# Kernel optimization log

Hardware: AMD Instinct MI355X
Metric: run time of the kernel (lower is better)

The kernel has to match this reference:

```python
import jax, jax.numpy as jnp
from jax import lax
import numpy as np

RNN = 512; FC = 512; COND = 128; FEAT = 80; NCLS = 256; HALF = RNN // 2
PAD = 2; SCALES = (5, 5, 11); MEL_T = 86  # -> 22550 output samples


def setup_inputs() -> dict:
    key = jax.random.key(0)
    ks = jax.random.split(key, 12)
    s = 0.05
    p = {"mels": jax.random.normal(ks[0], (1, FEAT, MEL_T), jnp.float32)}
    ch = FEAT
    for i, sc in enumerate(SCALES):
        k = 2 * sc + 1
        p[f"up_w{i}"] = jax.random.normal(ks[1 + i], (COND, ch, k), jnp.float32) * s
        p[f"up_b{i}"] = jnp.zeros((COND,), jnp.float32)
        ch = COND
    p["Wx"] = jax.random.normal(ks[4], (3 * RNN, 3 + COND), jnp.float32) * s
    p["bx"] = jnp.zeros((3 * RNN,), jnp.float32)
    p["Wh"] = jax.random.normal(ks[5], (3 * RNN, RNN), jnp.float32) * s
    p["bh"] = jnp.zeros((3 * RNN,), jnp.float32)
    p["O1w"] = jax.random.normal(ks[6], (FC, HALF), jnp.float32) * s
    p["O1b"] = jnp.zeros((FC,), jnp.float32)
    p["O2w"] = jax.random.normal(ks[7], (NCLS, FC), jnp.float32) * s
    p["O2b"] = jnp.zeros((NCLS,), jnp.float32)
    p["O3w"] = jax.random.normal(ks[8], (FC, HALF), jnp.float32) * s
    p["O3b"] = jnp.zeros((FC,), jnp.float32)
    p["O4w"] = jax.random.normal(ks[9], (NCLS, FC), jnp.float32) * s
    p["O4b"] = jnp.zeros((NCLS,), jnp.float32)
    return p


def _upsample(mels, ws, bs):
    # mels[:, :, excess_pad:-excess_pad] with excess_pad = PAD - 1 = 1
    x = mels[:, :, PAD - 1:-(PAD - 1)]
    for w, b, sc in zip(ws, bs, SCALES):
        k = 2 * sc + 1
        # ConvTranspose1d(stride=sc, kernel=k, padding=(3*sc-1)//2) as an
        # input-dilated conv: edge pad = k-1-torch_pad = (sc+1)//2
        e = k - 1 - (3 * sc - 1) // 2
        x = lax.conv_general_dilated(x, w, window_strides=(1,),
                                     padding=[(e, e)], lhs_dilation=(sc,),
                                     dimension_numbers=('NCH', 'OIH', 'NCH'))
        x = jax.nn.relu(x + b[None, :, None])
    return x[0, :, 1:-1].T  # [T, COND]


def _gru(inp, h, Wx, bx, Wh, bh):
    xg = Wx @ inp + bx
    hg = Wh @ h + bh
    xr, xz, xn = jnp.split(xg, 3)
    hr, hz, hn = jnp.split(hg, 3)
    r = jax.nn.sigmoid(xr + hr)
    z = jax.nn.sigmoid(xz + hz)
    n = jnp.tanh(xn + r * hn)
    return (1.0 - z) * n + z * h


def reference(mels, up_w0, up_b0, up_w1, up_b1, up_w2, up_b2,
              Wx, bx, Wh, bh, O1w, O1b, O2w, O2b, O3w, O3b, O4w, O4b):
    cond = _upsample(mels, (up_w0, up_w1, up_w2), (up_b0, up_b1, up_b2))
    zero = jnp.float32(0.0)

    def step(carry, m_t):
        h, c_val, f_val = carry
        # coarse pass: x = [c_{t-1}, f_{t-1}, 0]
        inp1 = jnp.concatenate([jnp.stack([c_val, f_val, zero]), m_t])
        h1 = _gru(inp1, h, Wx, bx, Wh, bh)
        oc = O2w @ jax.nn.relu(O1w @ h1[:HALF] + O1b) + O2b
        c_cat = jnp.argmax(oc).astype(jnp.float32)  # deterministic=True path
        c_new = c_cat / 127.5 - 1.0
        # fine pass: x = [c_{t-1}, f_{t-1}, c_t]
        inp2 = jnp.concatenate([jnp.stack([c_val, f_val, c_new]), m_t])
        h2 = _gru(inp2, h, Wx, bx, Wh, bh)
        of = O4w @ jax.nn.relu(O3w @ h2[HALF:] + O3b) + O4b
        f_cat = jnp.argmax(of).astype(jnp.float32)
        f_new = f_cat / 127.5 - 1.0
        sample = (c_cat * 256.0 + f_cat) / 32767.5 - 1.0
        return (h2, c_new, f_new), (sample, jnp.concatenate([oc, of]))

    init = (jnp.zeros((RNN,), jnp.float32), zero, zero)
    _, (samples, logits) = lax.scan(step, init, cond)
    return samples, logits  # [T], [T, 512]
```

## Files before the change

kernel.cpp:

```cpp
#include <hip/hip_runtime.h>
#include <math.h>

#define T_STEPS 22550
#define NWG 32
#define NTHR 256

typedef unsigned long long ull;

#define SL_H1   0
#define SL_O1   256
#define SL_AM1  768
#define SL_H2   800
#define SL_O3   1312
#define SL_AM2  1824
#define SL_END  1888

#define OF_SLOT  64
#define OF_AFTER (OF_SLOT + SL_END*2)
#define OF_BUFA  OF_AFTER
#define OF_BUFB  (OF_BUFA + 128*412)
#define OF_COND  (OF_BUFB + 128*2052)

__global__ void k_init(float* ws){
  int i = blockIdx.x*blockDim.x + threadIdx.x;
  ull* sl = (ull*)(ws + OF_SLOT);
  if (i < SL_END) __hip_atomic_store(&sl[i], 0ULL, __ATOMIC_RELAXED, __HIP_MEMORY_SCOPE_AGENT);
}

__global__ void k_upconv(const float* __restrict__ x, int instride, int inoff,
                         const float* __restrict__ w, const float* __restrict__ b,
                         float* __restrict__ y, int Cin, int Lin, int K, int sc, int e,
                         int Lout, int mode)
{
  int j = blockIdx.x*blockDim.x + threadIdx.x;
  int c = blockIdx.y;
  if (j >= Lout) return;
  float acc = b[c];
  int kstart = ((e - j) % sc + sc) % sc;
  for (int i = 0; i < Cin; ++i){
    const float* wci = w + (c*Cin + i)*K;
    const float* xi  = x + i*instride + inoff;
    for (int k = kstart; k < K; k += sc){
      int qd = j - e + k;
      if (qd >= 0){
        int qq = qd / sc;
        if (qq < Lin) acc += wci[k]*xi[qq];
      }
    }
  }
  acc = fmaxf(acc, 0.f);
  if (mode == 0) y[c*Lout + j] = acc;
  else { int t = j - 1; if (t >= 0 && t < T_STEPS) y[t*128 + c] = acc; }
}

__device__ __forceinline__ float sigm(float x){ return 1.f/(1.f + expf(-x)); }

__device__ __forceinline__ void pub64(ull* p, ull pk){
  (void)__hip_atomic_exchange(p, pk, __ATOMIC_RELAXED, __HIP_MEMORY_SCOPE_AGENT);
}
__device__ __forceinline__ ull ld64(ull* p){
  return __hip_atomic_load(p, __ATOMIC_RELAXED, __HIP_MEMORY_SCOPE_AGENT);
}
__device__ __forceinline__ float spin_data(ull* p, unsigned tag){
  ull pk = ld64(p);
  while ((unsigned)pk != tag) pk = ld64(p);
  return __uint_as_float((unsigned)(pk >> 32));
}
__device__ __forceinline__ ull spin_am(ull* p, unsigned tag){
  ull pk = ld64(p);
  while ((unsigned)(pk & 0xFFFFFFu) != tag) pk = ld64(p);
  return pk;
}
__device__ __forceinline__ ull pack_data(float v, unsigned tag){
  return ((ull)__float_as_uint(v) << 32) | (ull)tag;
}

__launch_bounds__(NTHR)
__global__ void k_wavernn(const float* __restrict__ Wx, const float* __restrict__ bx,
                          const float* __restrict__ Wh, const float* __restrict__ bh,
                          const float* __restrict__ O1w, const float* __restrict__ O1b,
                          const float* __restrict__ O2w, const float* __restrict__ O2b,
                          const float* __restrict__ O3w, const float* __restrict__ O3b,
                          const float* __restrict__ O4w, const float* __restrict__ O4b,
                          float* ws, float* __restrict__ out)
{
  __shared__ __align__(16) float h_s[512];
  __shared__ __align__(16) float m_s[128];
  __shared__ __align__(16) float h1c_s[256];
  __shared__ __align__(16) float o_s[512];
  __shared__ float hg_s[48], xgb_s[48], xg1_s[48];
  __shared__ float red_s[8], sc_s[8];
  __shared__ float wc0_s[48], wc1_s[48], wc2_s[48], bx_s[48], bh_s[48];

  const int tid = threadIdx.x, g = blockIdx.x;
  ull* sl = (ull*)(ws + OF_SLOT);
  const float* cond = ws + OF_COND;
  float* out_samp = out;
  float* out_log  = out + T_STEPS;

  if (tid < 48){
    int row = (tid>>4)*512 + g + 32*(tid&15);
    wc0_s[tid] = Wx[(size_t)row*131 + 0];
    wc1_s[tid] = Wx[(size_t)row*131 + 1];
    wc2_s[tid] = Wx[(size_t)row*131 + 2];
    bx_s[tid]  = bx[row];
    bh_s[tid]  = bh[row];
  }
  const int m16 = tid>>4, c16 = tid&15;
  const int rowO1 = g + 32*m16;
  float wO1r[16], wO3r[16];
  #pragma unroll
  for (int k=0;k<16;++k){
    wO1r[k] = O1w[(size_t)rowO1*256 + c16*16 + k];
    wO3r[k] = O3w[(size_t)rowO1*256 + c16*16 + k];
  }
  const float bO1r = O1b[rowO1], bO3r = O3b[rowO1];
  const int m8 = tid>>5, l32 = tid&31;
  const int row2 = g + 32*m8;
  float wO2r[16], wO4r[16];
  #pragma unroll
  for (int k=0;k<16;++k){
    wO2r[k] = O2w[(size_t)row2*512 + l32 + 32*k];
    wO4r[k] = O4w[(size_t)row2*512 + l32 + 32*k];
  }
  const float bO2 = O2b[row2], bO4 = O4b[row2];

  h_s[tid] = 0.f; h_s[tid+256] = 0.f;
  if (tid < 128) m_s[tid] = cond[tid];
  if (tid == 0){ sc_s[0] = 0.f; sc_s[1] = 0.f; }
  __syncthreads();

  #define COMPUTE_WX() do { \
    if (tid < 192){ \
      const int li_ = tid>>2, q_ = tid&3; \
      const int row_ = (li_>>4)*512 + g + 32*(li_&15); \
      const float* WxR = Wx + (size_t)row_*131 + 3; \
      float aX = 0.f; \
      _Pragma("unroll") \
      for (int kk=0; kk<32; ++kk){ \
        int f_ = q_*32 + ((kk + 8*q_) & 31); \
        aX += WxR[f_]*m_s[f_]; \
      } \
      aX += __shfl_xor(aX,1); aX += __shfl_xor(aX,2); \
      if (q_ == 0) xgb_s[li_] = aX + bx_s[li_]; \
    } } while(0)

  #define COMPUTE_WH() do { \
    if (tid < 192){ \
      const int li_ = tid>>2, q_ = tid&3; \
      const int row_ = (li_>>4)*512 + g + 32*(li_&15); \
      const float4* W4 = (const float4*)(Wh + (size_t)row_*512); \
      const float4* H4 = (const float4*)h_s; \
      float aH = 0.f; \
      _Pragma("unroll") \
      for (int kk=0; kk<32; ++kk){ \
        int f_ = q_*32 + ((kk + 2*q_) & 31); \
        float4 w = W4[f_], v = H4[f_]; \
        aH += w.x*v.x + w.y*v.y + w.z*v.z + w.w*v.w; \
      } \
      aH += __shfl_xor(aH,1); aH += __shfl_xor(aH,2); \
      if (q_ == 0) hg_s[li_] = aH + bh_s[li_]; \
    } } while(0)

  COMPUTE_WX();
  COMPUTE_WH();

  for (int t = 0; t < T_STEPS; ++t){
    const unsigned tag = (unsigned)(t + 1);
    __syncthreads();

    if (tid < 48) xg1_s[tid] = xgb_s[tid] + sc_s[0]*wc0_s[tid] + sc_s[1]*wc1_s[tid];
    if (tid < 128 && t + 1 < T_STEPS) m_s[tid] = cond[(size_t)(t+1)*128 + tid];
    __syncthreads();

    if (tid < 8){
      float r = sigm(xg1_s[tid]     + hg_s[tid]);
      float z = sigm(xg1_s[16+tid]  + hg_s[16+tid]);
      float n = tanhf(xg1_s[32+tid] + r*hg_s[32+tid]);
      float h1 = (1.f - z)*n + z*h_s[g + 32*tid];
      pub64(&sl[SL_H1 + g*8 + tid], pack_data(h1, tag));
    }
    h1c_s[tid] = spin_data(&sl[SL_H1 + (tid & 31)*8 + (tid >> 5)], tag);
    __syncthreads();

    {
      float acc = 0.f;
      #pragma unroll
      for (int k=0;k<16;++k) acc += wO1r[k]*h1c_s[c16*16 + k];
      acc += __shfl_xor(acc,1); acc += __shfl_xor(acc,2);
      acc += __shfl_xor(acc,4); acc += __shfl_xor(acc,8);
      if (c16 == 0) pub64(&sl[SL_O1 + g*16 + m16], pack_data(fmaxf(acc + bO1r, 0.f), tag));
    }
    o_s[tid]       = spin_data(&sl[SL_O1 + (tid & 31)*16 + (tid >> 5)], tag);
    o_s[tid + 256] = spin_data(&sl[SL_O1 + (tid & 31)*16 + (tid >> 5) + 8], tag);
    __syncthreads();

    {
      float acc = 0.f;
      #pragma unroll
      for (int k=0;k<16;++k) acc += wO2r[k]*o_s[l32 + 32*k];
      acc += __shfl_xor(acc,1); acc += __shfl_xor(acc,2); acc += __shfl_xor(acc,4);
      acc += __shfl_xor(acc,8); acc += __shfl_xor(acc,16);
      if (l32 == 0){ float v = acc + bO2; out_log[(size_t)t*512 + row2] = v; red_s[m8] = v; }
    }
    __syncthreads();
    if (tid == 0){
      float bv = red_s[0]; int bi = g;
      #pragma unroll
      for (int m=1;m<8;++m){ float v = red_s[m]; if (v > bv){ bv = v; bi = g + 32*m; } }
      pub64(&sl[SL_AM1 + g],
            ((ull)__float_as_uint(bv) << 32) | ((ull)(unsigned)bi << 24) | tag);
    }

    COMPUTE_WX();

    if (tid < 32){
      ull pk = spin_am(&sl[SL_AM1 + tid], tag);
      float bv = __uint_as_float((unsigned)(pk >> 32));
      int   bi = (int)((pk >> 24) & 0xFFu);
      #pragma unroll
      for (int off=16; off>=1; off>>=1){
        float ov = __shfl_xor(bv,off); int oi = __shfl_xor(bi,off);
        if (ov > bv || (ov == bv && oi < bi)){ bv = ov; bi = oi; }
      }
      if (tid == 0){ sc_s[2] = (float)bi; sc_s[3] = (float)bi/127.5f - 1.f; }
    }
    __syncthreads();

    if (tid < 16){
      float cn = sc_s[3];
      float r = sigm(xg1_s[tid]     + cn*wc2_s[tid]     + hg_s[tid]);
      float z = sigm(xg1_s[16+tid]  + cn*wc2_s[16+tid]  + hg_s[16+tid]);
      float n = tanhf(xg1_s[32+tid] + cn*wc2_s[32+tid]  + r*hg_s[32+tid]);
      float h2 = (1.f - z)*n + z*h_s[g + 32*tid];
      pub64(&sl[SL_H2 + g*16 + tid], pack_data(h2, tag));
    }
    __syncthreads();
    h_s[tid]       = spin_data(&sl[SL_H2 + (tid & 31)*16 + (tid >> 5)], tag);
    h_s[tid + 256] = spin_data(&sl[SL_H2 + (tid & 31)*16 + (tid >> 5) + 8], tag);
    __syncthreads();

    {
      float acc = 0.f;
      #pragma unroll
      for (int k=0;k<16;++k) acc += wO3r[k]*h_s[256 + c16*16 + k];
      acc += __shfl_xor(acc,1); acc += __shfl_xor(acc,2);
      acc += __shfl_xor(acc,4); acc += __shfl_xor(acc,8);
      if (c16 == 0) pub64(&sl[SL_O3 + g*16 + m16], pack_data(fmaxf(acc + bO3r, 0.f), tag));
    }
    o_s[tid]       = spin_data(&sl[SL_O3 + (tid & 31)*16 + (tid >> 5)], tag);
    o_s[tid + 256] = spin_data(&sl[SL_O3 + (tid & 31)*16 + (tid >> 5) + 8], tag);
    __syncthreads();

    {
      float acc = 0.f;
      #pragma unroll
      for (int k=0;k<16;++k) acc += wO4r[k]*o_s[l32 + 32*k];
      acc += __shfl_xor(acc,1); acc += __shfl_xor(acc,2); acc += __shfl_xor(acc,4);
      acc += __shfl_xor(acc,8); acc += __shfl_xor(acc,16);
      if (l32 == 0){ float v = acc + bO4; out_log[(size_t)t*512 + 256 + row2] = v; red_s[m8] = v; }
    }
    __syncthreads();
    if (tid == 0){
      float bv = red_s[0]; int bi = g;
      #pragma unroll
      for (int m=1;m<8;++m){ float v = red_s[m]; if (v > bv){ bv = v; bi = g + 32*m; } }
      pub64(&sl[SL_AM2 + (t & 1)*32 + g],
            ((ull)__float_as_uint(bv) << 32) | ((ull)(unsigned)bi << 24) | tag);
    }

    COMPUTE_WH();

    if (tid < 32){
      ull pk = spin_am(&sl[SL_AM2 + (t & 1)*32 + tid], tag);
      float bv = __uint_as_float((unsigned)(pk >> 32));
      int   bi = (int)((pk >> 24) & 0xFFu);
      #pragma unroll
      for (int off=16; off>=1; off>>=1){
        float ov = __shfl_xor(bv,off); int oi = __shfl_xor(bi,off);
        if (ov > bv || (ov == bv && oi < bi)){ bv = ov; bi = oi; }
      }
      if (tid == 0){
        sc_s[0] = sc_s[3];
        sc_s[1] = (float)bi/127.5f - 1.f;
        if (g == 0) out_samp[t] = (sc_s[2]*256.f + (float)bi)/32767.5f - 1.f;
      }
    }
  }
}

extern "C" void kernel_launch(void* const* d_in, const int* in_sizes, int n_in,
                              void* d_out, int out_size, void* d_ws, size_t ws_size,
                              hipStream_t stream)
{
  const float* mels  = (const float*)d_in[0];
  const float* up_w0 = (const float*)d_in[1]; const float* up_b0 = (const float*)d_in[2];
  const float* up_w1 = (const float*)d_in[3]; const float* up_b1 = (const float*)d_in[4];
  const float* up_w2 = (const float*)d_in[5]; const float* up_b2 = (const float*)d_in[6];
  const float* Wx  = (const float*)d_in[7];  const float* bx  = (const float*)d_in[8];
  const float* Wh  = (const float*)d_in[9];  const float* bh  = (const float*)d_in[10];
  const float* O1w = (const float*)d_in[11]; const float* O1b = (const float*)d_in[12];
  const float* O2w = (const float*)d_in[13]; const float* O2b = (const float*)d_in[14];
  const float* O3w = (const float*)d_in[15]; const float* O3b = (const float*)d_in[16];
  const float* O4w = (const float*)d_in[17]; const float* O4b = (const float*)d_in[18];
  float* ws  = (float*)d_ws;
  float* out = (float*)d_out;

  k_init<<<8, 256, 0, stream>>>(ws);

  k_upconv<<<dim3((412  +127)/128, 128), 128, 0, stream>>>(mels,        86,   1, up_w0, up_b0,
            ws+OF_BUFA,  80,   84, 11,  5, 3,   412, 0);
  k_upconv<<<dim3((2052 +127)/128, 128), 128, 0, stream>>>(ws+OF_BUFA, 412,   0, up_w1, up_b1,
            ws+OF_BUFB, 128,  412, 11,  5, 3,  2052, 0);
  k_upconv<<<dim3((22552+127)/128, 128), 128, 0, stream>>>(ws+OF_BUFB, 2052,  0, up_w2, up_b2,
            ws+OF_COND, 128, 2052, 23, 11, 6, 22552, 1);

  k_wavernn<<<NWG, NTHR, 0, stream>>>(Wx, bx, Wh, bh, O1w, O1b, O2w, O2b,
                                      O3w, O3b, O4w, O4b, ws, out);
}
```

Baseline: 343.3 ms.

## Publish GRU pre-gates once per step and replicate GRU/O1/O3 locally per workgroup

Each workgroup now publishes partial gate pre-activations (Wx·cond + c·w0 + Wh·h terms) for its rows once per step. Every workgroup gathers all 512 rows' pre-gates and locally finishes both GRU passes, folding in the f_{t-1} and c_t input columns itself. It also computes the full O1/O3 layers redundantly from global weights, removing the per-step h1, O1, h2 and O3 cross-workgroup exchanges. The fine-argmax consumption is deferred to the start of the next step. This cuts the number of global spin-wait rounds per step from about six to three. In exchange each workgroup does redundant O1/O3 matvecs with weights streamed from memory/cache each step, uses much more LDS, and polls 8 slots per thread.

```diff
diff --git a/kernel.cpp b/kernel.cpp
--- a/kernel.cpp
+++ b/kernel.cpp
@@ -7,13 +7,10 @@
 
 typedef unsigned long long ull;
 
-#define SL_H1   0
-#define SL_O1   256
-#define SL_AM1  768
-#define SL_H2   800
-#define SL_O3   1312
-#define SL_AM2  1824
-#define SL_END  1888
+#define SL_PRE  0
+#define SL_AM1  2048
+#define SL_AM2  2080
+#define SL_END  2144
 
 #define OF_SLOT  64
 #define OF_AFTER (OF_SLOT + SL_END*2)
@@ -61,11 +58,6 @@
 __device__ __forceinline__ ull ld64(ull* p){
   return __hip_atomic_load(p, __ATOMIC_RELAXED, __HIP_MEMORY_SCOPE_AGENT);
 }
-__device__ __forceinline__ float spin_data(ull* p, unsigned tag){
-  ull pk = ld64(p);
-  while ((unsigned)pk != tag) pk = ld64(p);
-  return __uint_as_float((unsigned)(pk >> 32));
-}
 __device__ __forceinline__ ull spin_am(ull* p, unsigned tag){
   ull pk = ld64(p);
   while ((unsigned)(pk & 0xFFFFFFu) != tag) pk = ld64(p);
@@ -86,11 +78,15 @@
 {
   __shared__ __align__(16) float h_s[512];
   __shared__ __align__(16) float m_s[128];
-  __shared__ __align__(16) float h1c_s[256];
+  __shared__ __align__(16) float h1_s[256];
   __shared__ __align__(16) float o_s[512];
-  __shared__ float hg_s[48], xgb_s[48], xg1_s[48];
+  __shared__ __align__(16) float pr_s[512], pz_s[512], pna_s[512], hn_s[512];
+  __shared__ __align__(16) float w1r_s[512], w1z_s[512], w1n_s[512];
+  __shared__ __align__(16) float w2r_s[512], w2z_s[512], w2n_s[512];
+  __shared__ __align__(16) float o1b_s[512], o3b_s[512];
+  __shared__ float hg_s[48], xgb_s[48];
   __shared__ float red_s[8], sc_s[8];
-  __shared__ float wc0_s[48], wc1_s[48], wc2_s[48], bx_s[48], bh_s[48];
+  __shared__ float wc0_s[48], bx_s[48], bh_s[48];
 
   const int tid = threadIdx.x, g = blockIdx.x;
   ull* sl = (ull*)(ws + OF_SLOT);
@@ -101,20 +97,19 @@
   if (tid < 48){
     int row = (tid>>4)*512 + g + 32*(tid&15);
     wc0_s[tid] = Wx[(size_t)row*131 + 0];
-    wc1_s[tid] = Wx[(size_t)row*131 + 1];
-    wc2_s[tid] = Wx[(size_t)row*131 + 2];
     bx_s[tid]  = bx[row];
     bh_s[tid]  = bh[row];
   }
-  const int m16 = tid>>4, c16 = tid&15;
-  const int rowO1 = g + 32*m16;
-  float wO1r[16], wO3r[16];
-  #pragma unroll
-  for (int k=0;k<16;++k){
-    wO1r[k] = O1w[(size_t)rowO1*256 + c16*16 + k];
-    wO3r[k] = O3w[(size_t)rowO1*256 + c16*16 + k];
-  }
-  const float bO1r = O1b[rowO1], bO3r = O3b[rowO1];
+  for (int e = tid; e < 512; e += NTHR){
+    w1r_s[e] = Wx[(size_t)e*131 + 1];
+    w1z_s[e] = Wx[(size_t)(512+e)*131 + 1];
+    w1n_s[e] = Wx[(size_t)(1024+e)*131 + 1];
+    w2r_s[e] = Wx[(size_t)e*131 + 2];
+    w2z_s[e] = Wx[(size_t)(512+e)*131 + 2];
+    w2n_s[e] = Wx[(size_t)(1024+e)*131 + 2];
+    o1b_s[e] = O1b[e];
+    o3b_s[e] = O3b[e];
+  }
   const int m8 = tid>>5, l32 = tid&31;
   const int row2 = g + 32*m8;
   float wO2r[16], wO4r[16];
@@ -124,10 +119,11 @@
     wO4r[k] = O4w[(size_t)row2*512 + l32 + 32*k];
   }
   const float bO2 = O2b[row2], bO4 = O4b[row2];
+  const int grp = tid>>4, c16 = tid&15;
 
   h_s[tid] = 0.f; h_s[tid+256] = 0.f;
   if (tid < 128) m_s[tid] = cond[tid];
-  if (tid == 0){ sc_s[0] = 0.f; sc_s[1] = 0.f; }
+  if (tid == 0){ sc_s[0] = 0.f; sc_s[2] = 0.f; sc_s[3] = 0.f; }
   __syncthreads();
 
   #define COMPUTE_WX() do { \
@@ -162,37 +158,95 @@
       if (q_ == 0) hg_s[li_] = aH + bh_s[li_]; \
     } } while(0)
 
+  #define PUB_PREGATES(TAGP) do { \
+    if (tid < 64){ \
+      const int i_ = tid>>2, c_ = tid&3; \
+      const int e_ = g + 32*i_; \
+      const float c0_ = sc_s[3]; \
+      float v_; \
+      if (c_ == 0)      v_ = xgb_s[i_]    + c0_*wc0_s[i_]    + hg_s[i_]; \
+      else if (c_ == 1) v_ = xgb_s[16+i_] + c0_*wc0_s[16+i_] + hg_s[16+i_]; \
+      else if (c_ == 2) v_ = xgb_s[32+i_] + c0_*wc0_s[32+i_]; \
+      else              v_ = hg_s[32+i_]; \
+      pub64(&sl[SL_PRE + e_*4 + c_], pack_data(v_, (TAGP))); \
+    } } while(0)
+
   COMPUTE_WX();
-  COMPUTE_WH();
+  if (tid < 48) hg_s[tid] = bh_s[tid];
+  __syncthreads();
+  PUB_PREGATES(1u);
 
   for (int t = 0; t < T_STEPS; ++t){
     const unsigned tag = (unsigned)(t + 1);
-    __syncthreads();
-
-    if (tid < 48) xg1_s[tid] = xgb_s[tid] + sc_s[0]*wc0_s[tid] + sc_s[1]*wc1_s[tid];
+
+    {
+      ull pk[8];
+      #pragma unroll
+      for (int c=0;c<4;++c){
+        pk[c]   = ld64(&sl[SL_PRE + tid*4 + c]);
+        pk[4+c] = ld64(&sl[SL_PRE + (tid+256)*4 + c]);
+      }
+      bool all;
+      do {
+        all = true;
+        #pragma unroll
+        for (int i=0;i<8;++i){
+          if ((unsigned)pk[i] != tag){
+            int slot = (i<4) ? (tid*4 + i) : ((tid+256)*4 + (i-4));
+            pk[i] = ld64(&sl[SL_PRE + slot]);
+            if ((unsigned)pk[i] != tag) all = false;
+          }
+        }
+      } while (!all);
+      pr_s[tid]      = __uint_as_float((unsigned)(pk[0] >> 32));
+      pz_s[tid]      = __uint_as_float((unsigned)(pk[1] >> 32));
+      pna_s[tid]     = __uint_as_float((unsigned)(pk[2] >> 32));
+      hn_s[tid]      = __uint_as_float((unsigned)(pk[3] >> 32));
+      pr_s[tid+256]  = __uint_as_float((unsigned)(pk[4] >> 32));
+      pz_s[tid+256]  = __uint_as_float((unsigned)(pk[5] >> 32));
+      pna_s[tid+256] = __uint_as_float((unsigned)(pk[6] >> 32));
+      hn_s[tid+256]  = __uint_as_float((unsigned)(pk[7] >> 32));
+    }
+    if (t > 0 && tid < 32){
+      ull pk = spin_am(&sl[SL_AM2 + ((t-1) & 1)*32 + tid], tag - 1);
+      float bv = __uint_as_float((unsigned)(pk >> 32));
+      int   bi = (int)((pk >> 24) & 0xFFu);
+      #pragma unroll
+      for (int off=16; off>=1; off>>=1){
+        float ov = __shfl_xor(bv,off); int oi = __shfl_xor(bi,off);
+        if (ov > bv || (ov == bv && oi < bi)){ bv = ov; bi = oi; }
+      }
+      if (tid == 0){
+        sc_s[0] = (float)bi/127.5f - 1.f;
+        if (g == 0) out_samp[t-1] = (sc_s[2]*256.f + (float)bi)/32767.5f - 1.f;
+      }
+    }
     if (tid < 128 && t + 1 < T_STEPS) m_s[tid] = cond[(size_t)(t+1)*128 + tid];
     __syncthreads();
 
-    if (tid < 8){
-      float r = sigm(xg1_s[tid]     + hg_s[tid]);
-      float z = sigm(xg1_s[16+tid]  + hg_s[16+tid]);
-      float n = tanhf(xg1_s[32+tid] + r*hg_s[32+tid]);
-      float h1 = (1.f - z)*n + z*h_s[g + 32*tid];
-      pub64(&sl[SL_H1 + g*8 + tid], pack_data(h1, tag));
-    }
-    h1c_s[tid] = spin_data(&sl[SL_H1 + (tid & 31)*8 + (tid >> 5)], tag);
-    __syncthreads();
-
-    {
+    {
+      const float f = sc_s[0];
+      float r = sigm(pr_s[tid]  + f*w1r_s[tid]);
+      float z = sigm(pz_s[tid]  + f*w1z_s[tid]);
+      float n = tanhf(pna_s[tid] + f*w1n_s[tid] + r*hn_s[tid]);
+      h1_s[tid] = (1.f - z)*n + z*h_s[tid];
+    }
+    __syncthreads();
+
+    for (int rr = 0; rr < 32; ++rr){
+      int row = grp*32 + rr;
+      const float4* W4 = (const float4*)(O1w + (size_t)row*256 + c16*16);
+      const float4* H4 = (const float4*)(h1_s + c16*16);
       float acc = 0.f;
       #pragma unroll
-      for (int k=0;k<16;++k) acc += wO1r[k]*h1c_s[c16*16 + k];
+      for (int k=0;k<4;++k){
+        float4 w = W4[k], v = H4[k];
+        acc += w.x*v.x + w.y*v.y + w.z*v.z + w.w*v.w;
+      }
       acc += __shfl_xor(acc,1); acc += __shfl_xor(acc,2);
       acc += __shfl_xor(acc,4); acc += __shfl_xor(acc,8);
-      if (c16 == 0) pub64(&sl[SL_O1 + g*16 + m16], pack_data(fmaxf(acc + bO1r, 0.f), tag));
-    }
-    o_s[tid]       = spin_data(&sl[SL_O1 + (tid & 31)*16 + (tid >> 5)], tag);
-    o_s[tid + 256] = spin_data(&sl[SL_O1 + (tid & 31)*16 + (tid >> 5) + 8], tag);
+      if (c16 == 0) o_s[row] = fmaxf(acc + o1b_s[row], 0.f);
+    }
     __syncthreads();
 
     {
@@ -212,8 +266,6 @@
             ((ull)__float_as_uint(bv) << 32) | ((ull)(unsigned)bi << 24) | tag);
     }
 
-    COMPUTE_WX();
-
     if (tid < 32){
       ull pk = spin_am(&sl[SL_AM1 + tid], tag);
       float bv = __uint_as_float((unsigned)(pk >> 32));
@@ -227,31 +279,34 @@
     }
     __syncthreads();
 
-    if (tid < 16){
-      float cn = sc_s[3];
-      float r = sigm(xg1_s[tid]     + cn*wc2_s[tid]     + hg_s[tid]);
-      float z = sigm(xg1_s[16+tid]  + cn*wc2_s[16+tid]  + hg_s[16+tid]);
-      float n = tanhf(xg1_s[32+tid] + cn*wc2_s[32+tid]  + r*hg_s[32+tid]);
-      float h2 = (1.f - z)*n + z*h_s[g + 32*tid];
-      pub64(&sl[SL_H2 + g*16 + tid], pack_data(h2, tag));
-    }
-    __syncthreads();
-    h_s[tid]       = spin_data(&sl[SL_H2 + (tid & 31)*16 + (tid >> 5)], tag);
-    h_s[tid + 256] = spin_data(&sl[SL_H2 + (tid & 31)*16 + (tid >> 5) + 8], tag);
-    __syncthreads();
-
-    {
+    {
+      const float f = sc_s[0], cn = sc_s[3];
+      #pragma unroll
+      for (int hh=0; hh<2; ++hh){
+        int e = tid + 256*hh;
+        float r = sigm(pr_s[e]  + f*w1r_s[e] + cn*w2r_s[e]);
+        float z = sigm(pz_s[e]  + f*w1z_s[e] + cn*w2z_s[e]);
+        float n = tanhf(pna_s[e] + f*w1n_s[e] + cn*w2n_s[e] + r*hn_s[e]);
+        h_s[e] = (1.f - z)*n + z*h_s[e];
+      }
+    }
+    __syncthreads();
+
+    for (int rr = 0; rr < 32; ++rr){
+      int row = grp*32 + rr;
+      const float4* W4 = (const float4*)(O3w + (size_t)row*256 + c16*16);
+      const float4* H4 = (const float4*)(h_s + 256 + c16*16);
       float acc = 0.f;
       #pragma unroll
-      for (int k=0;k<16;++k) acc += wO3r[k]*h_s[256 + c16*16 + k];
+      for (int k=0;k<4;++k){
+        float4 w = W4[k], v = H4[k];
+        acc += w.x*v.x + w.y*v.y + w.z*v.z + w.w*v.w;
+      }
       acc += __shfl_xor(acc,1); acc += __shfl_xor(acc,2);
       acc += __shfl_xor(acc,4); acc += __shfl_xor(acc,8);
-      if (c16 == 0) pub64(&sl[SL_O3 + g*16 + m16], pack_data(fmaxf(acc + bO3r, 0.f), tag));
-    }
-    o_s[tid]       = spin_data(&sl[SL_O3 + (tid & 31)*16 + (tid >> 5)], tag);
-    o_s[tid + 256] = spin_data(&sl[SL_O3 + (tid & 31)*16 + (tid >> 5) + 8], tag);
-    __syncthreads();
-
+      if (c16 == 0) o_s[row] = fmaxf(acc + o3b_s[row], 0.f);
+    }
+    __syncthreads();
     {
       float acc = 0.f;
       #pragma unroll
@@ -269,23 +324,22 @@
             ((ull)__float_as_uint(bv) << 32) | ((ull)(unsigned)bi << 24) | tag);
     }
 
+    COMPUTE_WX();
     COMPUTE_WH();
-
-    if (tid < 32){
-      ull pk = spin_am(&sl[SL_AM2 + (t & 1)*32 + tid], tag);
-      float bv = __uint_as_float((unsigned)(pk >> 32));
-      int   bi = (int)((pk >> 24) & 0xFFu);
-      #pragma unroll
-      for (int off=16; off>=1; off>>=1){
-        float ov = __shfl_xor(bv,off); int oi = __shfl_xor(bi,off);
-        if (ov > bv || (ov == bv && oi < bi)){ bv = ov; bi = oi; }
-      }
-      if (tid == 0){
-        sc_s[0] = sc_s[3];
-        sc_s[1] = (float)bi/127.5f - 1.f;
-        if (g == 0) out_samp[t] = (sc_s[2]*256.f + (float)bi)/32767.5f - 1.f;
-      }
-    }
+    __syncthreads();
+    if (t + 1 < T_STEPS) PUB_PREGATES((unsigned)(t + 2));
+  }
+
+  if (g == 0 && tid < 32){
+    ull pk = spin_am(&sl[SL_AM2 + ((T_STEPS-1) & 1)*32 + tid], (unsigned)T_STEPS);
+    float bv = __uint_as_float((unsigned)(pk >> 32));
+    int   bi = (int)((pk >> 24) & 0xFFu);
+    #pragma unroll
+    for (int off=16; off>=1; off>>=1){
+      float ov = __shfl_xor(bv,off); int oi = __shfl_xor(bi,off);
+      if (ov > bv || (ov == bv && oi < bi)){ bv = ov; bi = oi; }
+    }
+    if (tid == 0) out_samp[T_STEPS-1] = (sc_s[2]*256.f + (float)bi)/32767.5f - 1.f;
   }
 }
 
@@ -306,7 +360,7 @@
   float* ws  = (float*)d_ws;
   float* out = (float*)d_out;
 
-  k_init<<<8, 256, 0, stream>>>(ws);
+  k_init<<<(SL_END + 255)/256, 256, 0, stream>>>(ws);
 
   k_upconv<<<dim3((412  +127)/128, 128), 128, 0, stream>>>(mels,        86,   1, up_w0, up_b0,
             ws+OF_BUFA,  80,   84, 11,  5, 3,   412, 0);
```

Result: slower. 767.9 ms (+123.7%).
